# Kernel optimization log

Measured on AMD Instinct MI355X. Metric: run time of the kernel, lower is better.

The kernel has to match this reference:

```python
import jax, jax.numpy as jnp
import numpy as np

N_NODES = 50000
M_NEIGH = 16  # == ks
HID = 64
BATCH = 4


def setup_inputs() -> dict:
    key = jax.random.key(0)
    kx, ki = jax.random.split(key)
    x = jax.random.normal(kx, (BATCH, N_NODES, HID), dtype=jnp.float32)
    # values in [0, N_NODES] inclusive: N_NODES is the zero-padding row
    index = jax.random.randint(ki, (N_NODES, M_NEIGH), 0, N_NODES + 1, dtype=jnp.int64)
    return {"x": x, "index": index}


def reference(x, index):
    # x: [B, N, H]; index: [n, m] with values in [0, N] (N = padding zero row)
    B, N, H = x.shape
    n, m = index.shape
    x_pad = jnp.concatenate([x, jnp.zeros((B, 1, H), dtype=x.dtype)], axis=1)  # [B, N+1, H]
    gathered = x_pad[:, index.reshape(n * m), :]  # [B, n*m, H]
    # MaxPool1d(ks=m) over the gathered axis == segment max over neighbor groups
    out = gathered.reshape(B, n, m, H).max(axis=2)  # [B, n, H]
    return out
```

## Files before the change

### kernel.cpp

```cpp
#include <hip/hip_runtime.h>
#include <hip/hip_bf16.h>
#include <math.h>

#define N_NODES 50000
#define M_NEIGH 16
#define HID     64
#define BATCH   4

typedef float fvec4 __attribute__((ext_vector_type(4)));

#define SLAB_ROWS (N_NODES + 1)
#define SLAB_U4   ((size_t)SLAB_ROWS * 4)
#define SLAB_BYTES (SLAB_U4 * 16)
#define WS_NEED   (8 * SLAB_BYTES)

static __device__ __forceinline__ unsigned short f2bf_rne(float f) {
    union { float f; unsigned u; } v; v.f = f;
    unsigned r = v.u + 0x7fff + ((v.u >> 16) & 1);
    return (unsigned short)(r >> 16);
}
static __device__ __forceinline__ unsigned pack2(float a, float b) {
    return (unsigned)f2bf_rne(a) | ((unsigned)f2bf_rne(b) << 16);
}
static __device__ __forceinline__ float bf_lo(unsigned u) {
    union { unsigned u; float f; } v; v.u = u << 16; return v.f;
}
static __device__ __forceinline__ float bf_hi(unsigned u) {
    union { unsigned u; float f; } v; v.u = u & 0xffff0000u; return v.f;
}

#define CONV_MAIN (BATCH * N_NODES * 8)
__global__ __launch_bounds__(256) void convert_kernel(
    const fvec4* __restrict__ x, uint4* __restrict__ slabs)
{
    const int tid = blockIdx.x * 256 + threadIdx.x;
    if (tid < CONV_MAIN) {
        const int j8 = tid & 7;
        const int t2 = tid >> 3;
        const int n  = t2 % N_NODES;
        const int b  = t2 / N_NODES;
        const size_t src = ((size_t)b * N_NODES + n) * 16 + j8 * 2;
        const fvec4 f0 = x[src];
        const fvec4 f1 = x[src + 1];
        const int half = j8 >> 2;
        const int jq   = j8 & 3;
        uint4 u;
        u.x = pack2(f0.x, f0.y);
        u.y = pack2(f0.z, f0.w);
        u.z = pack2(f1.x, f1.y);
        u.w = pack2(f1.z, f1.w);
        slabs[(size_t)(half * 4 + b) * SLAB_U4 + (size_t)n * 4 + jq] = u;
    } else if (tid < CONV_MAIN + 32) {
        const int t = tid - CONV_MAIN;
        const int s = t >> 2, q = t & 3;
        slabs[(size_t)s * SLAB_U4 + (size_t)N_NODES * 4 + q] =
            make_uint4(0u, 0u, 0u, 0u);
    }
}

__global__ __launch_bounds__(256) void gather_max_kernel(
    const uint4* __restrict__ slabs,
    const int*   __restrict__ index,
    fvec4*       __restrict__ out)
{
    const int p     = blockIdx.x & 7;
    const int batch = p & 3;
    const int half  = p >> 2;
    const int wt    = (blockIdx.x >> 3) * 4 + (threadIdx.x >> 6);
    const int lane  = threadIdx.x & 63;
    const int q4    = lane & 3;
    const int li    = lane >> 2;
    const int nA    = wt * 32 + li;
    const int nB    = nA + 16;
    const bool vA   = nA < N_NODES;
    const bool vB   = nB < N_NODES;
    const int nAc   = vA ? nA : 0;
    const int nBc   = vB ? nB : 0;

    const uint4* slab = slabs + (size_t)p * SLAB_U4;
    const int4*  ipA  = (const int4*)(index + (size_t)nAc * M_NEIGH);
    const int4*  ipB  = (const int4*)(index + (size_t)nBc * M_NEIGH);

    int idxA[M_NEIGH], idxB[M_NEIGH];
#pragma unroll
    for (int mm = 0; mm < 4; ++mm) {
        const int4 rA = ipA[mm];
        const int4 rB = ipB[mm];
        idxA[mm * 4 + 0] = rA.x; idxA[mm * 4 + 1] = rA.y;
        idxA[mm * 4 + 2] = rA.z; idxA[mm * 4 + 3] = rA.w;
        idxB[mm * 4 + 0] = rB.x; idxB[mm * 4 + 1] = rB.y;
        idxB[mm * 4 + 2] = rB.z; idxB[mm * 4 + 3] = rB.w;
    }

    float aA0 = -INFINITY, aA1 = -INFINITY, aA2 = -INFINITY, aA3 = -INFINITY;
    float aA4 = -INFINITY, aA5 = -INFINITY, aA6 = -INFINITY, aA7 = -INFINITY;
    float aB0 = -INFINITY, aB1 = -INFINITY, aB2 = -INFINITY, aB3 = -INFINITY;
    float aB4 = -INFINITY, aB5 = -INFINITY, aB6 = -INFINITY, aB7 = -INFINITY;
#pragma unroll
    for (int m = 0; m < M_NEIGH; ++m) {
        const uint4 uA = slab[(size_t)idxA[m] * 4 + q4];
        const uint4 uB = slab[(size_t)idxB[m] * 4 + q4];
        aA0 = fmaxf(aA0, bf_lo(uA.x)); aA1 = fmaxf(aA1, bf_hi(uA.x));
        aA2 = fmaxf(aA2, bf_lo(uA.y)); aA3 = fmaxf(aA3, bf_hi(uA.y));
        aA4 = fmaxf(aA4, bf_lo(uA.z)); aA5 = fmaxf(aA5, bf_hi(uA.z));
        aA6 = fmaxf(aA6, bf_lo(uA.w)); aA7 = fmaxf(aA7, bf_hi(uA.w));
        aB0 = fmaxf(aB0, bf_lo(uB.x)); aB1 = fmaxf(aB1, bf_hi(uB.x));
        aB2 = fmaxf(aB2, bf_lo(uB.y)); aB3 = fmaxf(aB3, bf_hi(uB.y));
        aB4 = fmaxf(aB4, bf_lo(uB.z)); aB5 = fmaxf(aB5, bf_hi(uB.z));
        aB6 = fmaxf(aB6, bf_lo(uB.w)); aB7 = fmaxf(aB7, bf_hi(uB.w));
    }

    if (vA) {
        fvec4* o = &out[((size_t)batch * N_NODES + nA) * (HID / 4) + half * 8 + q4 * 2];
        __builtin_nontemporal_store((fvec4){aA0, aA1, aA2, aA3}, o);
        __builtin_nontemporal_store((fvec4){aA4, aA5, aA6, aA7}, o + 1);
    }
    if (vB) {
        fvec4* o = &out[((size_t)batch * N_NODES + nB) * (HID / 4) + half * 8 + q4 * 2];
        __builtin_nontemporal_store((fvec4){aB0, aB1, aB2, aB3}, o);
        __builtin_nontemporal_store((fvec4){aB4, aB5, aB6, aB7}, o + 1);
    }
}

__global__ __launch_bounds__(256) void pool_max_fallback(
    const fvec4* __restrict__ x, const int* __restrict__ index,
    fvec4* __restrict__ out)
{
    const int p     = blockIdx.x & 7;
    const int batch = p & 3;
    const int half  = p >> 2;
    const int group = blockIdx.x >> 3;
    const int wave  = threadIdx.x >> 6;
    const int lane  = threadIdx.x & 63;
    const int q8    = lane & 7;
    const int n     = group * 32 + wave * 8 + (lane >> 3);
    if (n >= N_NODES) return;

    const fvec4* xb = x + (size_t)batch * N_NODES * (HID / 4) + half * 8;
    const int* idx_ptr = index + (size_t)n * M_NEIGH;
    int idx[M_NEIGH];
#pragma unroll
    for (int m = 0; m < M_NEIGH; ++m) idx[m] = idx_ptr[m];

    fvec4 acc = (fvec4){-INFINITY, -INFINITY, -INFINITY, -INFINITY};
#pragma unroll
    for (int m = 0; m < M_NEIGH; ++m) {
        const int r  = idx[m];
        const int rc = r < N_NODES ? r : 0;
        fvec4 v = xb[(size_t)rc * (HID / 4) + q8];
        if (r >= N_NODES) v = (fvec4){0.f, 0.f, 0.f, 0.f};
        acc.x = fmaxf(acc.x, v.x); acc.y = fmaxf(acc.y, v.y);
        acc.z = fmaxf(acc.z, v.z); acc.w = fmaxf(acc.w, v.w);
    }
    __builtin_nontemporal_store(acc,
        &out[((size_t)batch * N_NODES + n) * (HID / 4) + half * 8 + q8]);
}

extern "C" void kernel_launch(void* const* d_in, const int* in_sizes, int n_in,
                              void* d_out, int out_size, void* d_ws, size_t ws_size,
                              hipStream_t stream) {
    const fvec4* x   = (const fvec4*)d_in[0];
    const int*   idx = (const int*)d_in[1];
    fvec4*       out = (fvec4*)d_out;

    if (ws_size >= WS_NEED) {
        uint4* slabs = (uint4*)d_ws;
        const int conv_blocks = (CONV_MAIN + 32 + 255) / 256;
        convert_kernel<<<conv_blocks, 256, 0, stream>>>(x, slabs);
        const int wts = (N_NODES + 31) / 32;
        const int bpp = (wts + 3) / 4;
        gather_max_kernel<<<bpp * 8, 256, 0, stream>>>(slabs, idx, out);
    } else {
        const int groups = (N_NODES + 31) / 32;
        pool_max_fallback<<<groups * 8, 256, 0, stream>>>(x, idx, out);
    }
}
```

Measured before the change: 130.8 us.

## Store full bf16 rows per batch and split gather work by node range

The bf16 workspace changes from eight half-row slabs (per batch and feature half) to four full-row slabs (one per batch), each 128 bytes per node. The gather kernel now has 8 lanes cover one full row, and the eight partitions are batch × node-half instead of batch × feature-half. Each random neighbour gather now fetches a contiguous 128-byte row instead of two separate 64-byte pieces, and each index row is read half as often. In exchange each partition touches a larger slab, which may reduce cache locality.

Result: no change. 129.5 us (-1.0%).

```diff
diff --git a/kernel.cpp b/kernel.cpp
--- a/kernel.cpp
+++ b/kernel.cpp
@@ -10,9 +10,9 @@
 typedef float fvec4 __attribute__((ext_vector_type(4)));
 
 #define SLAB_ROWS (N_NODES + 1)
-#define SLAB_U4   ((size_t)SLAB_ROWS * 4)
+#define SLAB_U4   ((size_t)SLAB_ROWS * 8)
 #define SLAB_BYTES (SLAB_U4 * 16)
-#define WS_NEED   (8 * SLAB_BYTES)
+#define WS_NEED   (4 * SLAB_BYTES)
 
 static __device__ __forceinline__ unsigned short f2bf_rne(float f) {
     union { float f; unsigned u; } v; v.f = f;
@@ -42,22 +42,21 @@
         const size_t src = ((size_t)b * N_NODES + n) * 16 + j8 * 2;
         const fvec4 f0 = x[src];
         const fvec4 f1 = x[src + 1];
-        const int half = j8 >> 2;
-        const int jq   = j8 & 3;
         uint4 u;
         u.x = pack2(f0.x, f0.y);
         u.y = pack2(f0.z, f0.w);
         u.z = pack2(f1.x, f1.y);
         u.w = pack2(f1.z, f1.w);
-        slabs[(size_t)(half * 4 + b) * SLAB_U4 + (size_t)n * 4 + jq] = u;
+        slabs[(size_t)b * SLAB_U4 + (size_t)n * 8 + j8] = u;
     } else if (tid < CONV_MAIN + 32) {
         const int t = tid - CONV_MAIN;
-        const int s = t >> 2, q = t & 3;
-        slabs[(size_t)s * SLAB_U4 + (size_t)N_NODES * 4 + q] =
+        const int s = t >> 3, q = t & 7;
+        slabs[(size_t)s * SLAB_U4 + (size_t)N_NODES * 8 + q] =
             make_uint4(0u, 0u, 0u, 0u);
     }
 }
 
+#define NODES_PER_PART 25000
 __global__ __launch_bounds__(256) void gather_max_kernel(
     const uint4* __restrict__ slabs,
     const int*   __restrict__ index,
@@ -65,21 +64,21 @@
 {
     const int p     = blockIdx.x & 7;
     const int batch = p & 3;
-    const int half  = p >> 2;
+    const int nbase = (p >> 2) * NODES_PER_PART;
     const int wt    = (blockIdx.x >> 3) * 4 + (threadIdx.x >> 6);
     const int lane  = threadIdx.x & 63;
-    const int q4    = lane & 3;
-    const int li    = lane >> 2;
-    const int nA    = wt * 32 + li;
-    const int nB    = nA + 16;
-    const bool vA   = nA < N_NODES;
-    const bool vB   = nB < N_NODES;
-    const int nAc   = vA ? nA : 0;
-    const int nBc   = vB ? nB : 0;
+    const int q8    = lane & 7;
+    const int li    = lane >> 3;
+    const int oA    = wt * 16 + li;
+    const int oB    = oA + 8;
+    const bool vA   = oA < NODES_PER_PART;
+    const bool vB   = oB < NODES_PER_PART;
+    const int nA    = nbase + (vA ? oA : 0);
+    const int nB    = nbase + (vB ? oB : 0);
 
-    const uint4* slab = slabs + (size_t)p * SLAB_U4;
-    const int4*  ipA  = (const int4*)(index + (size_t)nAc * M_NEIGH);
-    const int4*  ipB  = (const int4*)(index + (size_t)nBc * M_NEIGH);
+    const uint4* slab = slabs + (size_t)batch * SLAB_U4;
+    const int4*  ipA  = (const int4*)(index + (size_t)nA * M_NEIGH);
+    const int4*  ipB  = (const int4*)(index + (size_t)nB * M_NEIGH);
 
     int idxA[M_NEIGH], idxB[M_NEIGH];
 #pragma unroll
@@ -98,8 +97,8 @@
     float aB4 = -INFINITY, aB5 = -INFINITY, aB6 = -INFINITY, aB7 = -INFINITY;
 #pragma unroll
     for (int m = 0; m < M_NEIGH; ++m) {
-        const uint4 uA = slab[(size_t)idxA[m] * 4 + q4];
-        const uint4 uB = slab[(size_t)idxB[m] * 4 + q4];
+        const uint4 uA = slab[(size_t)idxA[m] * 8 + q8];
+        const uint4 uB = slab[(size_t)idxB[m] * 8 + q8];
         aA0 = fmaxf(aA0, bf_lo(uA.x)); aA1 = fmaxf(aA1, bf_hi(uA.x));
         aA2 = fmaxf(aA2, bf_lo(uA.y)); aA3 = fmaxf(aA3, bf_hi(uA.y));
         aA4 = fmaxf(aA4, bf_lo(uA.z)); aA5 = fmaxf(aA5, bf_hi(uA.z));
@@ -111,12 +110,12 @@
     }
 
     if (vA) {
-        fvec4* o = &out[((size_t)batch * N_NODES + nA) * (HID / 4) + half * 8 + q4 * 2];
+        fvec4* o = &out[((size_t)batch * N_NODES + nA) * (HID / 4) + q8 * 2];
         __builtin_nontemporal_store((fvec4){aA0, aA1, aA2, aA3}, o);
         __builtin_nontemporal_store((fvec4){aA4, aA5, aA6, aA7}, o + 1);
     }
     if (vB) {
-        fvec4* o = &out[((size_t)batch * N_NODES + nB) * (HID / 4) + half * 8 + q4 * 2];
+        fvec4* o = &out[((size_t)batch * N_NODES + nB) * (HID / 4) + q8 * 2];
         __builtin_nontemporal_store((fvec4){aB0, aB1, aB2, aB3}, o);
         __builtin_nontemporal_store((fvec4){aB4, aB5, aB6, aB7}, o + 1);
     }
@@ -167,7 +166,7 @@
         uint4* slabs = (uint4*)d_ws;
         const int conv_blocks = (CONV_MAIN + 32 + 255) / 256;
         convert_kernel<<<conv_blocks, 256, 0, stream>>>(x, slabs);
-        const int wts = (N_NODES + 31) / 32;
+        const int wts = (NODES_PER_PART + 15) / 16;
         const int bpp = (wts + 3) / 4;
         gather_max_kernel<<<bpp * 8, 256, 0, stream>>>(slabs, idx, out);
     } else {
```
